# Kernel tuning notes

Hardware: AMD Instinct MI355X
Metric: run time of the kernel (lower is better)

## Reference

```python
import jax, jax.numpy as jnp
import numpy as np

HEAD_NUM = 16
HEAD_DIM = 64
INPUT_DIM = 1024
OUTPUT_DIM = 1024
NEG_INF = -1e9  # value the torch code writes into masked score positions


def setup_inputs() -> dict:
    key = jax.random.key(0)
    k_x, k_v, k_w1, k_b1, k_w2, k_b2 = jax.random.split(key, 6)
    B, N = 2, 2048
    x = jax.random.normal(k_x, (B, N, INPUT_DIM), dtype=jnp.float32)
    vaild_num = jax.random.randint(k_v, (B,), 0, N, dtype=jnp.int32)
    s1 = 1.0 / np.sqrt(INPUT_DIM)
    s2 = 1.0 / np.sqrt(HEAD_NUM * HEAD_DIM)
    W_qkv = jax.random.uniform(k_w1, (INPUT_DIM, 3 * HEAD_NUM * HEAD_DIM), jnp.float32, -s1, s1)
    b_qkv = jax.random.uniform(k_b1, (3 * HEAD_NUM * HEAD_DIM,), jnp.float32, -s1, s1)
    W_proj = jax.random.uniform(k_w2, (HEAD_NUM * HEAD_DIM, OUTPUT_DIM), jnp.float32, -s2, s2)
    b_proj = jax.random.uniform(k_b2, (OUTPUT_DIM,), jnp.float32, -s2, s2)
    return {"x": x, "vaild_num": vaild_num, "W_qkv": W_qkv, "b_qkv": b_qkv,
            "W_proj": W_proj, "b_proj": b_proj}


def reference(x, vaild_num, W_qkv, b_qkv, W_proj, b_proj):
    B, N, _ = x.shape
    H, hd = HEAD_NUM, HEAD_DIM
    qkv = x @ W_qkv + b_qkv                      # [B, N, 3*H*hd]
    q, k, v = jnp.split(qkv, 3, axis=2)
    split = lambda t: t.reshape(B, N, H, hd).transpose(0, 2, 1, 3)  # [B, H, N, hd]
    q, k, v = split(q), split(k), split(v)
    score = jnp.einsum('bhqd,bhkd->bhqk', q, k) * (1.0 / np.sqrt(hd))
    # per-sample valid-length masking: rows >= v and cols >= v get -1e9
    valid = jnp.arange(N)[None, :] < vaild_num[:, None]            # [B, N]
    mask = valid[:, None, :, None] & valid[:, None, None, :]       # [B, 1, N, N]
    score = jnp.where(mask, score, NEG_INF)
    p = jax.nn.softmax(score, axis=-1)
    attn = jnp.einsum('bhqk,bhkd->bhqd', p, v)                     # [B, H, N, hd]
    attn = attn.transpose(0, 2, 1, 3).reshape(B, N, H * hd)
    return attn @ W_proj + b_proj
```

## Files before the change

kernel.cpp:

```cpp
#include <hip/hip_runtime.h>
#include <stdint.h>


typedef float    f32x4  __attribute__((ext_vector_type(4)));
typedef __bf16   bf16x8 __attribute__((ext_vector_type(8)));
typedef unsigned short u16x8 __attribute__((ext_vector_type(8)));
typedef unsigned short ushort_t;

#define HEADS 16
#define HDIM  64
#define NTOK  2048
#define BATCH 2
#define DIN   1024
#define D3    3072
#define MTOT  4096

__device__ __forceinline__ ushort_t f2bf(float x) {
  uint32_t u = __builtin_bit_cast(uint32_t, x);
  uint32_t r = (u + 0x7fffu + ((u >> 16) & 1u)) >> 16;
  return (ushort_t)r;
}
__device__ __forceinline__ float bf2f(ushort_t u) {
  return __builtin_bit_cast(float, (uint32_t)u << 16);
}

__device__ __forceinline__ void gld_lds16(const void* g, void* l) {
  auto gp = reinterpret_cast<const __attribute__((address_space(1))) uint32_t*>(
      reinterpret_cast<uintptr_t>(g));
  auto lp = reinterpret_cast<__attribute__((address_space(3))) uint32_t*>(
      reinterpret_cast<uintptr_t>(l));
  __builtin_amdgcn_global_load_lds(gp, lp, 16, 0, 0);
}

__global__ __launch_bounds__(256) void conv_bf16_kernel(
    const float* __restrict__ in, ushort_t* __restrict__ out, int n) {
  int i = (blockIdx.x * 256 + threadIdx.x) * 8;
  if (i >= n) return;
  float4 a = *(const float4*)(in + i);
  float4 b = *(const float4*)(in + i + 4);
  u16x8 v;
  v[0]=f2bf(a.x); v[1]=f2bf(a.y); v[2]=f2bf(a.z); v[3]=f2bf(a.w);
  v[4]=f2bf(b.x); v[5]=f2bf(b.y); v[6]=f2bf(b.z); v[7]=f2bf(b.w);
  *(u16x8*)(out + i) = v;
}

__global__ __launch_bounds__(256) void transpose_bf16_kernel(
    const float* __restrict__ in, ushort_t* __restrict__ out, int R, int C) {
  __shared__ float tile[64][65];
  const int r0 = blockIdx.y * 64, c0 = blockIdx.x * 64;
  const int t = threadIdx.x;
#pragma unroll
  for (int it = 0; it < 4; ++it) {
    int r = it * 16 + (t >> 4);
    int c = (t & 15) * 4;
    float4 v = *(const float4*)(in + (size_t)(r0 + r) * C + c0 + c);
    tile[r][c] = v.x; tile[r][c+1] = v.y; tile[r][c+2] = v.z; tile[r][c+3] = v.w;
  }
  __syncthreads();
#pragma unroll
  for (int it = 0; it < 2; ++it) {
    int idx = it * 2048 + t * 8;
    int c = idx >> 6;
    int r = idx & 63;
    u16x8 v;
#pragma unroll
    for (int j = 0; j < 8; ++j) v[j] = f2bf(tile[r + j][c]);
    *(u16x8*)(out + (size_t)(c0 + c) * R + r0 + r) = v;
  }
}

__device__ __forceinline__ void gemm_tile_mainloop(
    const ushort_t* __restrict__ A, const ushort_t* __restrict__ Bt,
    const int K, const int m0, const int n0,
    ushort_t* aT, ushort_t* bT, f32x4 (&acc)[4][4]) {
  const int t = threadIdx.x;
  const int l = t & 63;
  const int wr = t >> 7;
  const int wc = (t >> 6) & 1;

#pragma unroll
  for (int mi = 0; mi < 4; ++mi)
#pragma unroll
    for (int ni = 0; ni < 4; ++ni) acc[mi][ni] = f32x4{0.f, 0.f, 0.f, 0.f};

  for (int k0 = 0; k0 < K; k0 += 64) {
#pragma unroll
    for (int c = 0; c < 4; ++c) {
      const int lin = c * 4096 + t * 16;
      const int row = lin >> 7;
      const int scb = (lin & 127) ^ ((row & 7) << 4);
      const int ldso = (c * 4096 + (t >> 6) * 1024) >> 1;
      gld_lds16(A + (size_t)(m0 + row) * K + k0 + (scb >> 1), aT + ldso);
      gld_lds16(Bt + (size_t)(n0 + row) * K + k0 + (scb >> 1), bT + ldso);
    }
    __syncthreads();
#pragma unroll
    for (int ks = 0; ks < 2; ++ks) {
      bf16x8 af[4], bfr[4];
#pragma unroll
      for (int mi = 0; mi < 4; ++mi) {
        const int row = wr * 64 + mi * 16 + (l & 15);
        const int cb = (((l >> 4) << 4) + (ks << 6)) ^ ((row & 7) << 4);
        af[mi] = *(const bf16x8*)((const char*)aT + row * 128 + cb);
      }
#pragma unroll
      for (int ni = 0; ni < 4; ++ni) {
        const int row = wc * 64 + ni * 16 + (l & 15);
        const int cb = (((l >> 4) << 4) + (ks << 6)) ^ ((row & 7) << 4);
        bfr[ni] = *(const bf16x8*)((const char*)bT + row * 128 + cb);
      }
#pragma unroll
      for (int mi = 0; mi < 4; ++mi)
#pragma unroll
        for (int ni = 0; ni < 4; ++ni)
          acc[mi][ni] = __builtin_amdgcn_mfma_f32_16x16x32_bf16(
              af[mi], bfr[ni], acc[mi][ni], 0, 0, 0);
    }
    __syncthreads();
  }
}

__global__ __launch_bounds__(256) void gemm_qkv_kernel(
    const ushort_t* __restrict__ xb, const ushort_t* __restrict__ wT,
    const float* __restrict__ bias,
    ushort_t* __restrict__ Qb, ushort_t* __restrict__ Kb, ushort_t* __restrict__ Vt) {
  __shared__ __align__(16) ushort_t aT[128 * 64];
  __shared__ __align__(16) ushort_t bT[128 * 64];
  f32x4 acc[4][4];
  const int m0 = blockIdx.y * 128, n0 = blockIdx.x * 128;
  gemm_tile_mainloop(xb, wT, DIN, m0, n0, aT, bT, acc);

  const int t = threadIdx.x, l = t & 63;
  const int wr = t >> 7, wc = (t >> 6) & 1;
  const int which = n0 >> 10;
#pragma unroll
  for (int mi = 0; mi < 4; ++mi) {
#pragma unroll
    for (int ni = 0; ni < 4; ++ni) {
      const int n = n0 + wc * 64 + ni * 16 + (l & 15);
      const int h = (n >> 6) & 15, d = n & 63;
      const float bv = bias[n];
#pragma unroll
      for (int i = 0; i < 4; ++i) {
        const int m = m0 + wr * 64 + mi * 16 + ((l >> 4) << 2) + i;
        const int b = m >> 11, tok = m & 2047;
        const ushort_t val = f2bf(acc[mi][ni][i] + bv);
        const size_t bh = (size_t)((b << 4) + h);
        if (which == 0)      Qb[(bh * NTOK + tok) * HDIM + d] = val;
        else if (which == 1) Kb[(bh * NTOK + tok) * HDIM + d] = val;
        else                 Vt[(bh * HDIM + d) * NTOK + tok] = val;
      }
    }
  }
}

__global__ __launch_bounds__(256) void gemm_proj_kernel(
    const ushort_t* __restrict__ ab, const ushort_t* __restrict__ wT,
    const float* __restrict__ bias, float* __restrict__ out) {
  __shared__ __align__(16) ushort_t aT[128 * 64];
  __shared__ __align__(16) ushort_t bT[128 * 64];
  f32x4 acc[4][4];
  const int m0 = blockIdx.y * 128, n0 = blockIdx.x * 128;
  gemm_tile_mainloop(ab, wT, DIN, m0, n0, aT, bT, acc);

  const int t = threadIdx.x, l = t & 63;
  const int wr = t >> 7, wc = (t >> 6) & 1;
#pragma unroll
  for (int mi = 0; mi < 4; ++mi) {
#pragma unroll
    for (int ni = 0; ni < 4; ++ni) {
      const int n = n0 + wc * 64 + ni * 16 + (l & 15);
      const float bv = bias[n];
#pragma unroll
      for (int i = 0; i < 4; ++i) {
        const int m = m0 + wr * 64 + mi * 16 + ((l >> 4) << 2) + i;
        out[(size_t)m * 1024 + n] = acc[mi][ni][i] + bv;
      }
    }
  }
}

__global__ __launch_bounds__(256) void vmean_kernel(
    const ushort_t* __restrict__ Vt, ushort_t* __restrict__ vmean) {
  const int row = blockIdx.x * 4 + (threadIdx.x >> 6);
  const int l = threadIdx.x & 63;
  const ushort_t* src = Vt + (size_t)row * NTOK;
  float s = 0.f;
#pragma unroll
  for (int j = 0; j < 4; ++j) {
    u16x8 v = *(const u16x8*)(src + ((j << 6) + l) * 8);
#pragma unroll
    for (int k = 0; k < 8; ++k) s += bf2f(v[k]);
  }
#pragma unroll
  for (int d2 = 1; d2 < 64; d2 <<= 1) s += __shfl_xor(s, d2);
  if (l == 0) vmean[row] = f2bf(s * (1.0f / 2048.0f));
}

__global__ __launch_bounds__(256) void attn_kernel(
    const ushort_t* __restrict__ Qb, const ushort_t* __restrict__ Kb,
    const ushort_t* __restrict__ Vt, const ushort_t* __restrict__ vmean,
    const int* __restrict__ validp, ushort_t* __restrict__ ob) {
  __shared__ __align__(16) ushort_t kT[128 * 64];
  __shared__ __align__(16) ushort_t vT[64 * 128];
  __shared__ __align__(16) ushort_t pT[4][16 * 128];

  const int qt = blockIdx.x, h = blockIdx.y, b = blockIdx.z;
  const int q0 = qt << 6;
  const int valid = validp[b];
  const int t = threadIdx.x, w = t >> 6, l = t & 63;
  const size_t bh = (size_t)((b << 4) + h);
  const ushort_t* Qp = Qb + bh * (NTOK * HDIM);
  const ushort_t* Kp = Kb + bh * (NTOK * HDIM);
  const ushort_t* Vp = Vt + bh * (HDIM * NTOK);

  bf16x8 qf[2];
  {
    const int row = q0 + w * 16 + (l & 15);
    const ushort_t* s0 = Qp + (size_t)row * HDIM + ((l >> 4) << 3);
    qf[0] = *(const bf16x8*)(s0);
    qf[1] = *(const bf16x8*)(s0 + 32);
  }

  float mrow[4], lsum[4];
  f32x4 oacc[4];
#pragma unroll
  for (int i = 0; i < 4; ++i) { mrow[i] = -INFINITY; lsum[i] = 0.f; oacc[i] = f32x4{0.f,0.f,0.f,0.f}; }

  const int vlimit = (q0 < valid) ? valid : 0;
  for (int kv0 = 0; kv0 < vlimit; kv0 += 128) {
#pragma unroll
    for (int c = 0; c < 4; ++c) {
      const int lin = c * 4096 + t * 16;
      const int ldso = (c * 4096 + (t >> 6) * 1024) >> 1;
      {
        const int row = lin >> 7;
        const int scb = (lin & 127) ^ ((row & 7) << 4);
        gld_lds16(Kp + (size_t)(kv0 + row) * HDIM + (scb >> 1), kT + ldso);
      }
      {
        const int row = lin >> 8;
        const int scb = (lin & 255) ^ ((row & 7) << 4);
        gld_lds16(Vp + (size_t)row * NTOK + kv0 + (scb >> 1), vT + ldso);
      }
    }
    __syncthreads();

    f32x4 s[8];
#pragma unroll
    for (int blk = 0; blk < 8; ++blk) s[blk] = f32x4{0.f,0.f,0.f,0.f};
#pragma unroll
    for (int ks = 0; ks < 2; ++ks) {
#pragma unroll
      for (int blk = 0; blk < 8; ++blk) {
        const int kr = (blk << 4) + (l & 15);
        const int cb = (((l >> 4) << 4) + (ks << 6)) ^ ((kr & 7) << 4);
        bf16x8 kf = *(const bf16x8*)((const char*)kT + kr * 128 + cb);
        s[blk] = __builtin_amdgcn_mfma_f32_16x16x32_bf16(qf[ks], kf, s[blk], 0, 0, 0);
      }
    }

    float tmax[4];
#pragma unroll
    for (int i = 0; i < 4; ++i) tmax[i] = -1e30f;
#pragma unroll
    for (int blk = 0; blk < 8; ++blk) {
      const int col = kv0 + (blk << 4) + (l & 15);
      const bool ok = col < valid;
#pragma unroll
      for (int i = 0; i < 4; ++i) {
        float v = ok ? s[blk][i] * 0.125f : -1e30f;
        s[blk][i] = v;
        tmax[i] = fmaxf(tmax[i], v);
      }
    }
#pragma unroll
    for (int d2 = 1; d2 < 16; d2 <<= 1)
#pragma unroll
      for (int i = 0; i < 4; ++i) tmax[i] = fmaxf(tmax[i], __shfl_xor(tmax[i], d2));

    float mnew[4], rescale[4], tsum[4];
#pragma unroll
    for (int i = 0; i < 4; ++i) {
      mnew[i] = fmaxf(mrow[i], tmax[i]);
      rescale[i] = __expf(mrow[i] - mnew[i]);
      tsum[i] = 0.f;
    }

#pragma unroll
    for (int blk = 0; blk < 8; ++blk) {
#pragma unroll
      for (int i = 0; i < 4; ++i) {
        const float p = __expf(s[blk][i] - mnew[i]);
        tsum[i] += p;
        const int pr = ((l >> 4) << 2) + i;
        const int cb = (((blk << 4) + (l & 15)) << 1) ^ ((pr & 7) << 4);
        *(ushort_t*)((char*)pT[w] + pr * 256 + cb) = f2bf(p);
      }
    }
#pragma unroll
    for (int d2 = 1; d2 < 16; d2 <<= 1)
#pragma unroll
      for (int i = 0; i < 4; ++i) tsum[i] += __shfl_xor(tsum[i], d2);
#pragma unroll
    for (int i = 0; i < 4; ++i) {
      lsum[i] = lsum[i] * rescale[i] + tsum[i];
      mrow[i] = mnew[i];
    }
#pragma unroll
    for (int dblk = 0; dblk < 4; ++dblk)
#pragma unroll
      for (int i = 0; i < 4; ++i) oacc[dblk][i] *= rescale[i];

#pragma unroll
    for (int ks = 0; ks < 4; ++ks) {
      const int pr = l & 15;
      const int cba = (((l >> 4) << 4) + (ks << 6)) ^ ((pr & 7) << 4);
      bf16x8 pf = *(const bf16x8*)((const char*)pT[w] + pr * 256 + cba);
#pragma unroll
      for (int dblk = 0; dblk < 4; ++dblk) {
        const int vr = (dblk << 4) + (l & 15);
        const int cbb = (((l >> 4) << 4) + (ks << 6)) ^ ((vr & 7) << 4);
        bf16x8 vf = *(const bf16x8*)((const char*)vT + vr * 256 + cbb);
        oacc[dblk] = __builtin_amdgcn_mfma_f32_16x16x32_bf16(pf, vf, oacc[dblk], 0, 0, 0);
      }
    }
    __syncthreads();
  }

  if (q0 < valid) {
#pragma unroll
    for (int dblk = 0; dblk < 4; ++dblk) {
#pragma unroll
      for (int i = 0; i < 4; ++i) {
        const int row = q0 + w * 16 + ((l >> 4) << 2) + i;
        if (row < valid) {
          const int d = (dblk << 4) + (l & 15);
          ob[((size_t)(b * NTOK) + row) * 1024 + (h << 6) + d] =
              f2bf(oacc[dblk][i] / lsum[i]);
        }
      }
    }
  }
  for (int it = 0; it < 16; ++it) {
    const int idx = it * 256 + t;
    const int row = q0 + (idx >> 6);
    if (row >= valid) {
      const int d = idx & 63;
      ob[((size_t)(b * NTOK) + row) * 1024 + (h << 6) + d] = vmean[(bh << 6) + d];
    }
  }
}

extern "C" void kernel_launch(void* const* d_in, const int* in_sizes, int n_in,
                              void* d_out, int out_size, void* d_ws, size_t ws_size,
                              hipStream_t stream) {
  (void)in_sizes; (void)n_in; (void)out_size; (void)ws_size;
  const float* x      = (const float*)d_in[0];
  const int*   validp = (const int*)d_in[1];
  const float* W_qkv  = (const float*)d_in[2];
  const float* b_qkv  = (const float*)d_in[3];
  const float* W_proj = (const float*)d_in[4];
  const float* b_proj = (const float*)d_in[5];
  float* out = (float*)d_out;

  ushort_t* xb     = (ushort_t*)d_ws;
  ushort_t* wqkvT  = xb + 4194304;
  ushort_t* wprojT = wqkvT + 3145728;
  ushort_t* Qb     = wprojT + 1048576;
  ushort_t* Kb     = Qb + 4194304;
  ushort_t* Vt     = Kb + 4194304;
  ushort_t* ab     = Vt + 4194304;
  ushort_t* vm     = ab + 4194304;

  conv_bf16_kernel<<<2048, 256, 0, stream>>>(x, xb, 4194304);
  transpose_bf16_kernel<<<dim3(48, 16), 256, 0, stream>>>(W_qkv, wqkvT, 1024, 3072);
  transpose_bf16_kernel<<<dim3(16, 16), 256, 0, stream>>>(W_proj, wprojT, 1024, 1024);
  gemm_qkv_kernel<<<dim3(24, 32), 256, 0, stream>>>(xb, wqkvT, b_qkv, Qb, Kb, Vt);
  vmean_kernel<<<512, 256, 0, stream>>>(Vt, vm);
  attn_kernel<<<dim3(32, 16, 2), 256, 0, stream>>>(Qb, Kb, Vt, vm, validp, ab);
  gemm_proj_kernel<<<dim3(8, 32), 256, 0, stream>>>(ab, wprojT, b_proj, out);
}
```

Measured before the change: 245.0 us.

## Rewrite attention kernel with per-wave 32x32 MFMA tiles and register-resident softmax

The attention kernel moves from 16x16x32 MFMAs with K/V staged through LDS and block barriers to per-wave 32-query tiles using 32x32x16 MFMAs. K and V fragments are loaded straight from global memory into registers, P stays in registers via packed bf16 conversion and lane shuffles instead of an LDS round trip, softmax uses exp2 with a folded scale, and the rescale is skipped when no row max changes. This removes LDS traffic and __syncthreads stalls at the cost of redundant global K/V loads across the four waves and fewer, larger blocks (128 queries each). The output is staged through LDS for vectorised stores, and the mean-V fill for invalid rows is merged into the same store.

```diff
diff --git a/kernel.cpp b/kernel.cpp
--- a/kernel.cpp
+++ b/kernel.cpp
@@ -3,9 +3,12 @@
 
 
 typedef float    f32x4  __attribute__((ext_vector_type(4)));
+typedef float    f32x16 __attribute__((ext_vector_type(16)));
 typedef __bf16   bf16x8 __attribute__((ext_vector_type(8)));
 typedef unsigned short u16x8 __attribute__((ext_vector_type(8)));
+typedef unsigned int   u32x4 __attribute__((ext_vector_type(4)));
 typedef unsigned short ushort_t;
+typedef unsigned int   u32;
 
 #define HEADS 16
 #define HDIM  64
@@ -15,6 +18,8 @@
 #define D3    3072
 #define MTOT  4096
 
+#define SC 0.18033688f
+
 __device__ __forceinline__ ushort_t f2bf(float x) {
   uint32_t u = __builtin_bit_cast(uint32_t, x);
   uint32_t r = (u + 0x7fffu + ((u >> 16) & 1u)) >> 16;
@@ -22,6 +27,11 @@
 }
 __device__ __forceinline__ float bf2f(ushort_t u) {
   return __builtin_bit_cast(float, (uint32_t)u << 16);
+}
+__device__ __forceinline__ u32 cvt_pk_bf16(float lo, float hi) {
+  u32 r;
+  asm("v_cvt_pk_bf16_f32 %0, %1, %2" : "=v"(r) : "v"(lo), "v"(hi));
+  return r;
 }
 
 __device__ __forceinline__ void gld_lds16(const void* g, void* l) {
@@ -201,154 +211,168 @@
     const ushort_t* __restrict__ Qb, const ushort_t* __restrict__ Kb,
     const ushort_t* __restrict__ Vt, const ushort_t* __restrict__ vmean,
     const int* __restrict__ validp, ushort_t* __restrict__ ob) {
-  __shared__ __align__(16) ushort_t kT[128 * 64];
-  __shared__ __align__(16) ushort_t vT[64 * 128];
-  __shared__ __align__(16) ushort_t pT[4][16 * 128];
-
-  const int qt = blockIdx.x, h = blockIdx.y, b = blockIdx.z;
-  const int q0 = qt << 6;
+  __shared__ ushort_t ot_all[4][32 * 68];
+
+  const int h = blockIdx.y, b = blockIdx.z;
   const int valid = validp[b];
   const int t = threadIdx.x, w = t >> 6, l = t & 63;
+  const int lq = l & 31, hi = l >> 5;
+  const int wq0 = (blockIdx.x << 7) + (w << 5);
   const size_t bh = (size_t)((b << 4) + h);
   const ushort_t* Qp = Qb + bh * (NTOK * HDIM);
   const ushort_t* Kp = Kb + bh * (NTOK * HDIM);
   const ushort_t* Vp = Vt + bh * (HDIM * NTOK);
 
-  bf16x8 qf[2];
-  {
-    const int row = q0 + w * 16 + (l & 15);
-    const ushort_t* s0 = Qp + (size_t)row * HDIM + ((l >> 4) << 3);
-    qf[0] = *(const bf16x8*)(s0);
-    qf[1] = *(const bf16x8*)(s0 + 32);
-  }
-
-  float mrow[4], lsum[4];
-  f32x4 oacc[4];
-#pragma unroll
-  for (int i = 0; i < 4; ++i) { mrow[i] = -INFINITY; lsum[i] = 0.f; oacc[i] = f32x4{0.f,0.f,0.f,0.f}; }
-
-  const int vlimit = (q0 < valid) ? valid : 0;
-  for (int kv0 = 0; kv0 < vlimit; kv0 += 128) {
-#pragma unroll
-    for (int c = 0; c < 4; ++c) {
-      const int lin = c * 4096 + t * 16;
-      const int ldso = (c * 4096 + (t >> 6) * 1024) >> 1;
+  f32x16 oacc[2];
+#pragma unroll
+  for (int db = 0; db < 2; ++db)
+#pragma unroll
+    for (int r = 0; r < 16; ++r) oacc[db][r] = 0.f;
+  float m_run = -INFINITY, lsum = 0.f;
+
+  if (wq0 < valid) {
+    bf16x8 qf[4];
+    const ushort_t* qbase = Qp + (size_t)(wq0 + lq) * HDIM + (hi << 3);
+#pragma unroll
+    for (int ks = 0; ks < 4; ++ks) qf[ks] = *(const bf16x8*)(qbase + (ks << 4));
+
+    const int nt = (valid + 63) >> 6;
+    for (int tt = 0; tt < nt; ++tt) {
+      const int kv0 = tt << 6;
+
+      bf16x8 kf[2][4];
+#pragma unroll
+      for (int kb2 = 0; kb2 < 2; ++kb2) {
+        const ushort_t* kbase = Kp + (size_t)(kv0 + (kb2 << 5) + lq) * HDIM + (hi << 3);
+#pragma unroll
+        for (int ks = 0; ks < 4; ++ks) kf[kb2][ks] = *(const bf16x8*)(kbase + (ks << 4));
+      }
+      bf16x8 vf[2][2][2];
+#pragma unroll
+      for (int db = 0; db < 2; ++db) {
+        const ushort_t* vbase = Vp + (size_t)((db << 5) + lq) * NTOK + kv0 + (hi << 3);
+#pragma unroll
+        for (int kb2 = 0; kb2 < 2; ++kb2)
+#pragma unroll
+          for (int k2 = 0; k2 < 2; ++k2)
+            vf[db][kb2][k2] = *(const bf16x8*)(vbase + (kb2 << 5) + (k2 << 4));
+      }
+
+      f32x16 st[2];
+#pragma unroll
+      for (int kb2 = 0; kb2 < 2; ++kb2)
+#pragma unroll
+        for (int r = 0; r < 16; ++r) st[kb2][r] = 0.f;
+      __builtin_amdgcn_s_setprio(1);
+#pragma unroll
+      for (int ks = 0; ks < 4; ++ks) {
+        st[0] = __builtin_amdgcn_mfma_f32_32x32x16_bf16(kf[0][ks], qf[ks], st[0], 0, 0, 0);
+        st[1] = __builtin_amdgcn_mfma_f32_32x32x16_bf16(kf[1][ks], qf[ks], st[1], 0, 0, 0);
+      }
+      __builtin_amdgcn_s_setprio(0);
+
+      if (kv0 + 64 > valid) {
+#pragma unroll
+        for (int kb2 = 0; kb2 < 2; ++kb2)
+#pragma unroll
+          for (int r = 0; r < 16; ++r) {
+            const int k = kv0 + (kb2 << 5) + (r & 3) + ((r >> 2) << 3) + (hi << 2);
+            if (k >= valid) st[kb2][r] = -1e30f;
+          }
+      }
+
+      float pm;
       {
-        const int row = lin >> 7;
-        const int scb = (lin & 127) ^ ((row & 7) << 4);
-        gld_lds16(Kp + (size_t)(kv0 + row) * HDIM + (scb >> 1), kT + ldso);
-      }
-      {
-        const int row = lin >> 8;
-        const int scb = (lin & 255) ^ ((row & 7) << 4);
-        gld_lds16(Vp + (size_t)row * NTOK + kv0 + (scb >> 1), vT + ldso);
-      }
-    }
-    __syncthreads();
-
-    f32x4 s[8];
-#pragma unroll
-    for (int blk = 0; blk < 8; ++blk) s[blk] = f32x4{0.f,0.f,0.f,0.f};
-#pragma unroll
-    for (int ks = 0; ks < 2; ++ks) {
-#pragma unroll
-      for (int blk = 0; blk < 8; ++blk) {
-        const int kr = (blk << 4) + (l & 15);
-        const int cb = (((l >> 4) << 4) + (ks << 6)) ^ ((kr & 7) << 4);
-        bf16x8 kf = *(const bf16x8*)((const char*)kT + kr * 128 + cb);
-        s[blk] = __builtin_amdgcn_mfma_f32_16x16x32_bf16(qf[ks], kf, s[blk], 0, 0, 0);
-      }
-    }
-
-    float tmax[4];
-#pragma unroll
-    for (int i = 0; i < 4; ++i) tmax[i] = -1e30f;
-#pragma unroll
-    for (int blk = 0; blk < 8; ++blk) {
-      const int col = kv0 + (blk << 4) + (l & 15);
-      const bool ok = col < valid;
-#pragma unroll
-      for (int i = 0; i < 4; ++i) {
-        float v = ok ? s[blk][i] * 0.125f : -1e30f;
-        s[blk][i] = v;
-        tmax[i] = fmaxf(tmax[i], v);
-      }
-    }
-#pragma unroll
-    for (int d2 = 1; d2 < 16; d2 <<= 1)
-#pragma unroll
-      for (int i = 0; i < 4; ++i) tmax[i] = fmaxf(tmax[i], __shfl_xor(tmax[i], d2));
-
-    float mnew[4], rescale[4], tsum[4];
-#pragma unroll
-    for (int i = 0; i < 4; ++i) {
-      mnew[i] = fmaxf(mrow[i], tmax[i]);
-      rescale[i] = __expf(mrow[i] - mnew[i]);
-      tsum[i] = 0.f;
-    }
-
-#pragma unroll
-    for (int blk = 0; blk < 8; ++blk) {
-#pragma unroll
-      for (int i = 0; i < 4; ++i) {
-        const float p = __expf(s[blk][i] - mnew[i]);
-        tsum[i] += p;
-        const int pr = ((l >> 4) << 2) + i;
-        const int cb = (((blk << 4) + (l & 15)) << 1) ^ ((pr & 7) << 4);
-        *(ushort_t*)((char*)pT[w] + pr * 256 + cb) = f2bf(p);
-      }
-    }
-#pragma unroll
-    for (int d2 = 1; d2 < 16; d2 <<= 1)
-#pragma unroll
-      for (int i = 0; i < 4; ++i) tsum[i] += __shfl_xor(tsum[i], d2);
-#pragma unroll
-    for (int i = 0; i < 4; ++i) {
-      lsum[i] = lsum[i] * rescale[i] + tsum[i];
-      mrow[i] = mnew[i];
-    }
-#pragma unroll
-    for (int dblk = 0; dblk < 4; ++dblk)
-#pragma unroll
-      for (int i = 0; i < 4; ++i) oacc[dblk][i] *= rescale[i];
-
-#pragma unroll
-    for (int ks = 0; ks < 4; ++ks) {
-      const int pr = l & 15;
-      const int cba = (((l >> 4) << 4) + (ks << 6)) ^ ((pr & 7) << 4);
-      bf16x8 pf = *(const bf16x8*)((const char*)pT[w] + pr * 256 + cba);
-#pragma unroll
-      for (int dblk = 0; dblk < 4; ++dblk) {
-        const int vr = (dblk << 4) + (l & 15);
-        const int cbb = (((l >> 4) << 4) + (ks << 6)) ^ ((vr & 7) << 4);
-        bf16x8 vf = *(const bf16x8*)((const char*)vT + vr * 256 + cbb);
-        oacc[dblk] = __builtin_amdgcn_mfma_f32_16x16x32_bf16(pf, vf, oacc[dblk], 0, 0, 0);
-      }
-    }
-    __syncthreads();
-  }
-
-  if (q0 < valid) {
-#pragma unroll
-    for (int dblk = 0; dblk < 4; ++dblk) {
-#pragma unroll
-      for (int i = 0; i < 4; ++i) {
-        const int row = q0 + w * 16 + ((l >> 4) << 2) + i;
-        if (row < valid) {
-          const int d = (dblk << 4) + (l & 15);
-          ob[((size_t)(b * NTOK) + row) * 1024 + (h << 6) + d] =
-              f2bf(oacc[dblk][i] / lsum[i]);
+        float a8[8];
+#pragma unroll
+        for (int i = 0; i < 8; ++i)
+          a8[i] = fmaxf(fmaxf(st[0][i], st[0][i + 8]), fmaxf(st[1][i], st[1][i + 8]));
+        float b4[4];
+#pragma unroll
+        for (int i = 0; i < 4; ++i) b4[i] = fmaxf(a8[i], a8[i + 4]);
+        pm = fmaxf(fmaxf(b4[0], b4[1]), fmaxf(b4[2], b4[3]));
+      }
+      pm = fmaxf(pm, __shfl_xor(pm, 32));
+
+      if (__any(pm > m_run)) {
+        const float mnew = fmaxf(m_run, pm);
+        const float rs = exp2f((m_run - mnew) * SC);
+        lsum *= rs;
+#pragma unroll
+        for (int db = 0; db < 2; ++db)
+#pragma unroll
+          for (int r = 0; r < 16; ++r) oacc[db][r] *= rs;
+        m_run = mnew;
+      }
+
+      const float mc = m_run * SC;
+      float pp[2][16];
+      float ts4[4] = {0.f, 0.f, 0.f, 0.f};
+#pragma unroll
+      for (int kb2 = 0; kb2 < 2; ++kb2)
+#pragma unroll
+        for (int r = 0; r < 16; ++r) {
+          const float e = exp2f(fmaf(st[kb2][r], SC, -mc));
+          pp[kb2][r] = e;
+          ts4[r & 3] += e;
         }
-      }
-    }
-  }
-  for (int it = 0; it < 16; ++it) {
-    const int idx = it * 256 + t;
-    const int row = q0 + (idx >> 6);
-    if (row >= valid) {
-      const int d = idx & 63;
-      ob[((size_t)(b * NTOK) + row) * 1024 + (h << 6) + d] = vmean[(bh << 6) + d];
-    }
+      float tsum = (ts4[0] + ts4[1]) + (ts4[2] + ts4[3]);
+      tsum += __shfl_xor(tsum, 32);
+      lsum += tsum;
+
+      bf16x8 pb[2][2];
+#pragma unroll
+      for (int kb2 = 0; kb2 < 2; ++kb2) {
+        u32 c[8];
+#pragma unroll
+        for (int m2 = 0; m2 < 8; ++m2)
+          c[m2] = cvt_pk_bf16(pp[kb2][2 * m2], pp[kb2][2 * m2 + 1]);
+        const u32 x1 = (u32)__shfl_xor((int)(hi ? c[0] : c[2]), 32);
+        const u32 x2 = (u32)__shfl_xor((int)(hi ? c[1] : c[3]), 32);
+        const u32 x3 = (u32)__shfl_xor((int)(hi ? c[4] : c[6]), 32);
+        const u32 x4 = (u32)__shfl_xor((int)(hi ? c[5] : c[7]), 32);
+        u32x4 w0, w1;
+        w0[0] = hi ? x1 : c[0];  w0[1] = hi ? x2 : c[1];
+        w0[2] = hi ? c[2] : x1;  w0[3] = hi ? c[3] : x2;
+        w1[0] = hi ? x3 : c[4];  w1[1] = hi ? x4 : c[5];
+        w1[2] = hi ? c[6] : x3;  w1[3] = hi ? c[7] : x4;
+        pb[kb2][0] = __builtin_bit_cast(bf16x8, w0);
+        pb[kb2][1] = __builtin_bit_cast(bf16x8, w1);
+      }
+
+      __builtin_amdgcn_s_setprio(1);
+#pragma unroll
+      for (int db = 0; db < 2; ++db)
+#pragma unroll
+        for (int kb2 = 0; kb2 < 2; ++kb2)
+#pragma unroll
+          for (int k2 = 0; k2 < 2; ++k2)
+            oacc[db] = __builtin_amdgcn_mfma_f32_32x32x16_bf16(
+                vf[db][kb2][k2], pb[kb2][k2], oacc[db], 0, 0, 0);
+      __builtin_amdgcn_s_setprio(0);
+    }
+  }
+
+  const float inv = (lsum > 0.f) ? 1.0f / lsum : 0.f;
+  ushort_t* ot = ot_all[w];
+#pragma unroll
+  for (int db = 0; db < 2; ++db)
+#pragma unroll
+    for (int r = 0; r < 16; ++r) {
+      const int d = (r & 3) + ((r >> 2) << 3) + (hi << 2) + (db << 5);
+      ot[lq * 68 + d] = f2bf(oacc[db][r] * inv);
+    }
+  asm volatile("s_waitcnt lgkmcnt(0)" ::: "memory");
+#pragma unroll
+  for (int it = 0; it < 8; ++it) {
+    const int c2 = it * 64 + l;
+    const int row = c2 >> 4;
+    const int ch = c2 & 15;
+    const uint2 vo = *(const uint2*)((const char*)ot + row * 136 + ch * 8);
+    const uint2 vm = *(const uint2*)(vmean + (bh << 6) + ch * 4);
+    const int grow = wq0 + row;
+    const uint2 sel = (grow < valid) ? vo : vm;
+    *(uint2*)(ob + ((size_t)(b * NTOK) + grow) * 1024 + (h << 6) + ch * 4) = sel;
   }
 }
 
@@ -378,6 +402,6 @@
   transpose_bf16_kernel<<<dim3(16, 16), 256, 0, stream>>>(W_proj, wprojT, 1024, 1024);
   gemm_qkv_kernel<<<dim3(24, 32), 256, 0, stream>>>(xb, wqkvT, b_qkv, Qb, Kb, Vt);
   vmean_kernel<<<512, 256, 0, stream>>>(Vt, vm);
-  attn_kernel<<<dim3(32, 16, 2), 256, 0, stream>>>(Qb, Kb, Vt, vm, validp, ab);
+  attn_kernel<<<dim3(16, 16, 2), 256, 0, stream>>>(Qb, Kb, Vt, vm, validp, ab);
   gemm_proj_kernel<<<dim3(8, 32), 256, 0, stream>>>(ab, wprojT, b_proj, out);
 }
```

After: 246.2 us. No clear change (+0.5%).
